# Optimization experiments

Measured on AMD Instinct MI355X. Metric: run time of the kernel, lower is better.

The kernel has to match this reference:

```python
import jax, jax.numpy as jnp
import numpy as np

K_SEL = 16  # number of selected positions per distribution
EPS = 1e-20


def setup_inputs() -> dict:
    key = jax.random.key(0)
    k1, k2 = jax.random.split(key)
    d0, vocab, BS = 64, 2048, 32
    logits = jax.random.normal(k1, (d0, vocab), dtype=jnp.float32)
    # Gumbel noise exactly as in the dense branch: -0.001*log(-log(U+eps)+eps)
    u = jax.random.uniform(k2, (BS, d0, vocab), dtype=jnp.float32)
    gn = -0.001 * jnp.log(-jnp.log(u + EPS) + EPS)
    return {"logits": logits, "gn": gn}


def reference(logits, gn):
    # logits: [d0, V], gn: [BS, d0, V]
    vocab = logits.shape[-1]
    perturbed = logits[None, :, :] + gn                     # [BS, d0, V]
    # top-k indices of perturbed logits, then top-k of the indices themselves
    # (sorts the selected indices descending); reverse -> ascending order.
    _, idx = jax.lax.top_k(perturbed, K_SEL)                # [BS, d0, k]
    idx_sorted, _ = jax.lax.top_k(idx, K_SEL)               # descending indices
    topk = idx_sorted[..., ::-1]                            # ascending
    hard = jax.nn.one_hot(topk, vocab, dtype=logits.dtype)  # [BS, d0, k, V]
    # exclusive cumsum mask along the k axis
    cum_mask = jnp.cumsum(hard, axis=-2) - hard             # [BS, d0, k, V]
    Temp = 1.0
    prob_exp = jnp.exp(logits)[None, :, None, :]            # [1, d0, 1, V]
    soft = jax.nn.sigmoid(
        (jnp.log(prob_exp * (1.0 - cum_mask + EPS)) + gn[:, :, None, :]) / Temp
    )                                                        # [BS, d0, k, V]
    return jax.lax.stop_gradient(hard - soft) + soft
```

## Files before the change

### kernel.cpp

```cpp
#include <hip/hip_runtime.h>
#include <math.h>

#define K_SEL   16
#define VOCAB   2048
#define NROWS   2048
#define THREADS 256

__global__ __launch_bounds__(THREADS) void topk_onehot_kernel(
    const float* __restrict__ logits,
    const float* __restrict__ gn,
    float* __restrict__ out)
{
    const int row  = blockIdx.x;
    const int d0   = row & 63;
    const int tid  = threadIdx.x;
    const int lane = tid & 63;
    const int wid  = tid >> 6;

    const int c0 = tid * 4;
    const int c1 = 1024 + tid * 4;

    const float4 g0 = *reinterpret_cast<const float4*>(gn + (size_t)row * VOCAB + c0);
    const float4 g1 = *reinterpret_cast<const float4*>(gn + (size_t)row * VOCAB + c1);
    const float4 l0 = *reinterpret_cast<const float4*>(logits + (size_t)d0 * VOCAB + c0);
    const float4 l1 = *reinterpret_cast<const float4*>(logits + (size_t)d0 * VOCAB + c1);

    float v[8];
    v[0] = l0.x + g0.x; v[1] = l0.y + g0.y; v[2] = l0.z + g0.z; v[3] = l0.w + g0.w;
    v[4] = l1.x + g1.x; v[5] = l1.y + g1.y; v[6] = l1.z + g1.z; v[7] = l1.w + g1.w;

    __shared__ float swv[4];
    __shared__ int   swi[4];
    __shared__ int   sel[K_SEL];
    __shared__ int   sorted[K_SEL];

    for (int k = 0; k < K_SEL; ++k) {
        float bestv = v[0];
        int   besti = c0;
        #pragma unroll
        for (int j = 1; j < 8; ++j) {
            const int cj = (j < 4) ? (c0 + j) : (c1 + (j - 4));
            if (v[j] > bestv) { bestv = v[j]; besti = cj; }
        }
        #pragma unroll
        for (int off = 1; off < 64; off <<= 1) {
            const float ov = __shfl_xor(bestv, off);
            const int   oi = __shfl_xor(besti, off);
            if (ov > bestv || (ov == bestv && oi < besti)) { bestv = ov; besti = oi; }
        }
        if (lane == 0) { swv[wid] = bestv; swi[wid] = besti; }
        __syncthreads();
        if (tid == 0) {
            float bv = swv[0]; int bi = swi[0];
            #pragma unroll
            for (int w = 1; w < 4; ++w) {
                if (swv[w] > bv || (swv[w] == bv && swi[w] < bi)) { bv = swv[w]; bi = swi[w]; }
            }
            sel[k] = bi;
        }
        __syncthreads();
        const int widx = sel[k];
        #pragma unroll
        for (int j = 0; j < 8; ++j) {
            const int cj = (j < 4) ? (c0 + j) : (c1 + (j - 4));
            if (cj == widx) v[j] = -INFINITY;
        }
    }

    if (tid < K_SEL) {
        const int my = sel[tid];
        int rank = 0;
        #pragma unroll
        for (int j = 0; j < K_SEL; ++j) rank += (sel[j] < my) ? 1 : 0;
        sorted[rank] = my;
    }
    __syncthreads();

    float* orow = out + (size_t)row * K_SEL * VOCAB;
    #pragma unroll
    for (int k = 0; k < K_SEL; ++k) {
        const int one = sorted[k];
        float4 a, b;
        a.x = (one == c0 + 0) ? 1.0f : 0.0f;
        a.y = (one == c0 + 1) ? 1.0f : 0.0f;
        a.z = (one == c0 + 2) ? 1.0f : 0.0f;
        a.w = (one == c0 + 3) ? 1.0f : 0.0f;
        b.x = (one == c1 + 0) ? 1.0f : 0.0f;
        b.y = (one == c1 + 1) ? 1.0f : 0.0f;
        b.z = (one == c1 + 2) ? 1.0f : 0.0f;
        b.w = (one == c1 + 3) ? 1.0f : 0.0f;
        *reinterpret_cast<float4*>(orow + (size_t)k * VOCAB + c0) = a;
        *reinterpret_cast<float4*>(orow + (size_t)k * VOCAB + c1) = b;
    }
}

extern "C" void kernel_launch(void* const* d_in, const int* in_sizes, int n_in,
                              void* d_out, int out_size, void* d_ws, size_t ws_size,
                              hipStream_t stream) {
    const float* logits = (const float*)d_in[0];
    const float* gn     = (const float*)d_in[1];
    float* out          = (float*)d_out;

    hipLaunchKernelGGL(topk_onehot_kernel, dim3(NROWS), dim3(THREADS), 0, stream,
                       logits, gn, out);
}
```

Before: 56.20 us.

## Use one wavefront per row with cached local max and overlapped zero-fill

Each row is now handled by a single 64-lane wavefront holding 32 values per lane, which removes the shared-memory cross-wave reduction and both __syncthreads per selection step. Each lane keeps its local maximum cached, and only the lane that owned the winner rescans its values after a selection. Zero-filling of the output rows is issued during the selection loop so the stores overlap the shuffles. The ones are scattered afterwards, with the rank computed in registers. In exchange there are fewer threads per block, higher register pressure, and the correctness of the one-hot writes depends on the explicit vmcnt wait ordering them after the zero stores.

```diff
diff --git a/kernel.cpp b/kernel.cpp
--- a/kernel.cpp
+++ b/kernel.cpp
@@ -4,93 +4,75 @@
 #define K_SEL   16
 #define VOCAB   2048
 #define NROWS   2048
-#define THREADS 256
 
-__global__ __launch_bounds__(THREADS) void topk_onehot_kernel(
+__global__ __launch_bounds__(64) void topk_onehot_kernel(
     const float* __restrict__ logits,
     const float* __restrict__ gn,
     float* __restrict__ out)
 {
     const int row  = blockIdx.x;
     const int d0   = row & 63;
-    const int tid  = threadIdx.x;
-    const int lane = tid & 63;
-    const int wid  = tid >> 6;
+    const int lane = threadIdx.x;
 
-    const int c0 = tid * 4;
-    const int c1 = 1024 + tid * 4;
+    const float* grow = gn     + (size_t)row * VOCAB;
+    const float* lrow = logits + (size_t)d0  * VOCAB;
+    float*       orow = out    + (size_t)row * (K_SEL * VOCAB);
 
-    const float4 g0 = *reinterpret_cast<const float4*>(gn + (size_t)row * VOCAB + c0);
-    const float4 g1 = *reinterpret_cast<const float4*>(gn + (size_t)row * VOCAB + c1);
-    const float4 l0 = *reinterpret_cast<const float4*>(logits + (size_t)d0 * VOCAB + c0);
-    const float4 l1 = *reinterpret_cast<const float4*>(logits + (size_t)d0 * VOCAB + c1);
+    float v[32];
+    #pragma unroll
+    for (int seg = 0; seg < 8; ++seg) {
+        const int c = seg * 256 + lane * 4;
+        const float4 g = *reinterpret_cast<const float4*>(grow + c);
+        const float4 l = *reinterpret_cast<const float4*>(lrow + c);
+        v[seg * 4 + 0] = l.x + g.x;
+        v[seg * 4 + 1] = l.y + g.y;
+        v[seg * 4 + 2] = l.z + g.z;
+        v[seg * 4 + 3] = l.w + g.w;
+    }
 
-    float v[8];
-    v[0] = l0.x + g0.x; v[1] = l0.y + g0.y; v[2] = l0.z + g0.z; v[3] = l0.w + g0.w;
-    v[4] = l1.x + g1.x; v[5] = l1.y + g1.y; v[6] = l1.z + g1.z; v[7] = l1.w + g1.w;
+    float lv = v[0]; int ls = 0;
+    #pragma unroll
+    for (int i = 1; i < 32; ++i) { if (v[i] > lv) { lv = v[i]; ls = i; } }
 
-    __shared__ float swv[4];
-    __shared__ int   swi[4];
-    __shared__ int   sel[K_SEL];
-    __shared__ int   sorted[K_SEL];
+    const float4 z4 = make_float4(0.f, 0.f, 0.f, 0.f);
+    int sel[K_SEL];
 
+    #pragma unroll
     for (int k = 0; k < K_SEL; ++k) {
-        float bestv = v[0];
-        int   besti = c0;
         #pragma unroll
-        for (int j = 1; j < 8; ++j) {
-            const int cj = (j < 4) ? (c0 + j) : (c1 + (j - 4));
-            if (v[j] > bestv) { bestv = v[j]; besti = cj; }
+        for (int seg = 0; seg < 8; ++seg) {
+            *reinterpret_cast<float4*>(orow + (size_t)k * VOCAB + seg * 256 + lane * 4) = z4;
         }
+        float bv = lv;
+        int   bc = ((ls >> 2) << 8) + lane * 4 + (ls & 3);
         #pragma unroll
         for (int off = 1; off < 64; off <<= 1) {
-            const float ov = __shfl_xor(bestv, off);
-            const int   oi = __shfl_xor(besti, off);
-            if (ov > bestv || (ov == bestv && oi < besti)) { bestv = ov; besti = oi; }
+            const float ov = __shfl_xor(bv, off);
+            const int   oc = __shfl_xor(bc, off);
+            if (ov > bv || (ov == bv && oc < bc)) { bv = ov; bc = oc; }
         }
-        if (lane == 0) { swv[wid] = bestv; swi[wid] = besti; }
-        __syncthreads();
-        if (tid == 0) {
-            float bv = swv[0]; int bi = swi[0];
+        sel[k] = bc;
+        if (lane == ((bc >> 2) & 63)) {
+            const int s = (((bc >> 8) & 7) << 2) | (bc & 3);
+            lv = -INFINITY; ls = 0;
             #pragma unroll
-            for (int w = 1; w < 4; ++w) {
-                if (swv[w] > bv || (swv[w] == bv && swi[w] < bi)) { bv = swv[w]; bi = swi[w]; }
+            for (int i = 0; i < 32; ++i) {
+                if (i == s) v[i] = -INFINITY;
+                if (v[i] > lv) { lv = v[i]; ls = i; }
             }
-            sel[k] = bi;
-        }
-        __syncthreads();
-        const int widx = sel[k];
-        #pragma unroll
-        for (int j = 0; j < 8; ++j) {
-            const int cj = (j < 4) ? (c0 + j) : (c1 + (j - 4));
-            if (cj == widx) v[j] = -INFINITY;
         }
     }
 
-    if (tid < K_SEL) {
-        const int my = sel[tid];
-        int rank = 0;
-        #pragma unroll
-        for (int j = 0; j < K_SEL; ++j) rank += (sel[j] < my) ? 1 : 0;
-        sorted[rank] = my;
-    }
-    __syncthreads();
+    asm volatile("s_waitcnt vmcnt(0)" ::: "memory");
 
-    float* orow = out + (size_t)row * K_SEL * VOCAB;
     #pragma unroll
     for (int k = 0; k < K_SEL; ++k) {
-        const int one = sorted[k];
-        float4 a, b;
-        a.x = (one == c0 + 0) ? 1.0f : 0.0f;
-        a.y = (one == c0 + 1) ? 1.0f : 0.0f;
-        a.z = (one == c0 + 2) ? 1.0f : 0.0f;
-        a.w = (one == c0 + 3) ? 1.0f : 0.0f;
-        b.x = (one == c1 + 0) ? 1.0f : 0.0f;
-        b.y = (one == c1 + 1) ? 1.0f : 0.0f;
-        b.z = (one == c1 + 2) ? 1.0f : 0.0f;
-        b.w = (one == c1 + 3) ? 1.0f : 0.0f;
-        *reinterpret_cast<float4*>(orow + (size_t)k * VOCAB + c0) = a;
-        *reinterpret_cast<float4*>(orow + (size_t)k * VOCAB + c1) = b;
+        int r = 0;
+        #pragma unroll
+        for (int j = 0; j < K_SEL; ++j) r += (sel[j] < sel[k]) ? 1 : 0;
+        if (lane == ((sel[k] >> 2) & 63)) {
+            orow[(size_t)r * VOCAB + sel[k]] = 1.0f;
+        }
     }
 }
 
@@ -101,6 +83,6 @@
     const float* gn     = (const float*)d_in[1];
     float* out          = (float*)d_out;
 
-    hipLaunchKernelGGL(topk_onehot_kernel, dim3(NROWS), dim3(THREADS), 0, stream,
+    hipLaunchKernelGGL(topk_onehot_kernel, dim3(NROWS), dim3(64), 0, stream,
                        logits, gn, out);
 }
```

Measured after the change: 51.93 us. 1.08x faster.
